# Kernel optimization log

Measured on AMD Instinct MI355X. Metric: run time of the kernel, lower is better.

The kernel has to match this reference:

```python
import jax, jax.numpy as jnp
import numpy as np

B, L, H, D = 4, 2048, 12, 64
CHUNK = 128  # chunk size for the causal linear-attention scan
EPS = 1e-6


def setup_inputs() -> dict:
    key = jax.random.key(0)
    kq, kk, kv = jax.random.split(key, 3)
    return {
        "q": jax.random.normal(kq, (B, L, H, D), jnp.float32),
        "k": jax.random.normal(kk, (B, L, H, D), jnp.float32),
        "v": jax.random.normal(kv, (B, L, H, D), jnp.float32),
    }


def _phi(x):
    # elu feature map: elu(x) + 1 (strictly positive)
    return jax.nn.elu(x) + 1.0


def _causal_linear(q, k, v):
    """Chunked causal linear attention numerator.
    out[l] = q[l] @ sum_{s<=l} k[s] (x) v[s].  q,k,v: [N,L,H,D]."""
    n, l, h, d = q.shape
    g = l // CHUNK
    qc = q.reshape(n, g, CHUNK, h, d)
    kc = k.reshape(n, g, CHUNK, h, d)
    vc = v.reshape(n, g, CHUNK, h, d)
    # per-chunk kv outer-product sums -> [N, G, H, D, M]
    kv = jnp.einsum('ngchd,ngchm->nghdm', kc, vc)
    # exclusive prefix sum over chunks (state entering each chunk)
    s_incl = jnp.cumsum(kv, axis=1)
    s_excl = jnp.concatenate([jnp.zeros_like(s_incl[:, :1]), s_incl[:, :-1]], axis=1)
    inter = jnp.einsum('ngchd,nghdm->ngchm', qc, s_excl)
    # intra-chunk causal part
    scores = jnp.einsum('ngchd,ngshd->ngchs', qc, kc)  # [N,G,C,H,C]
    mask = jnp.tril(jnp.ones((CHUNK, CHUNK), scores.dtype))  # s <= c
    scores = scores * mask.reshape(1, 1, CHUNK, 1, CHUNK)
    intra = jnp.einsum('ngchs,ngshm->ngchm', scores, vc)
    return (inter + intra).reshape(n, l, h, -1)


def reference(q, k, v):
    qf = _phi(q)
    kf = _phi(k)
    # normalizer z[n,l,h] = q[l] . cumsum_s<=l k[s]
    z = jnp.einsum('nlhd,nlhd->nlh', qf, jnp.cumsum(kf, axis=1)) + EPS
    num = _causal_linear(qf, kf, v)
    return num / z[..., None]
```

## Files before the change

kernel.cpp:

```cpp
#include <hip/hip_runtime.h>

#define NB 4
#define LL 2048
#define NH 12
#define DD 64
#define CB 128
#define NG (LL/CB)
#define NBH (NB*NH)
#define ST_BYTES (DD*DD*2)
#define KS_BASE_BYTES ((size_t)NBH*NG*ST_BYTES)

typedef short bf16x8 __attribute__((ext_vector_type(8)));
typedef float f32x4  __attribute__((ext_vector_type(4)));

#define SWZ8(row, x)  ((x) ^ (((row) & 7) << 4))
#define SWZ16(row, x) ((x) ^ (((row) & 15) << 4))

__device__ __forceinline__ float phi(float x) {
    return x > 0.0f ? x + 1.0f : __expf(x);
}
__device__ __forceinline__ unsigned f2bf1(float x) {
    union { float f; unsigned u; } v; v.f = x;
    return (v.u + 0x7FFFu + ((v.u >> 16) & 1u)) >> 16;
}
__device__ __forceinline__ unsigned packbf(float a, float b) {
    return f2bf1(a) | (f2bf1(b) << 16);
}
__device__ __forceinline__ float bf2f(unsigned short u) {
    union { unsigned u; float f; } v; v.u = ((unsigned)u) << 16; return v.f;
}
__device__ __forceinline__ void addbf8(float* run, uint4 a) {
    const unsigned u[4] = {a.x, a.y, a.z, a.w};
    #pragma unroll
    for (int i = 0; i < 4; ++i) {
        run[2*i+0] += bf2f((unsigned short)(u[i] & 0xffffu));
        run[2*i+1] += bf2f((unsigned short)(u[i] >> 16));
    }
}
__device__ __forceinline__ uint4 pack8(const float* run) {
    uint4 s;
    s.x = packbf(run[0], run[1]); s.y = packbf(run[2], run[3]);
    s.z = packbf(run[4], run[5]); s.w = packbf(run[6], run[7]);
    return s;
}

__global__ __launch_bounds__(256) void la_chunk_sums(
    const float* __restrict__ kin, const float* __restrict__ vin,
    char* __restrict__ wsb)
{
    __shared__ __align__(16) char sm[32768];
    const int bid = blockIdx.x;
    const int g = bid & (NG-1);
    const int h = (bid >> 4) % NH;
    const int n = bid / (NG*NH);
    const int t = threadIdx.x;
    const int l0 = g * CB;
    const int w = t >> 6, l = t & 63, gq = l >> 4, c16 = l & 15;

    #pragma unroll
    for (int p = 0; p < 8; ++p) {
        const int i = p*256 + t;
        const int r = i >> 4, c4 = i & 15;
        const size_t gidx = ((size_t)((n*LL + l0 + r)*NH + h))*DD + c4*4;
        float4 kk = *(const float4*)(kin + gidx);
        float4 vl = *(const float4*)(vin + gidx);
        const float kf[4] = {phi(kk.x), phi(kk.y), phi(kk.z), phi(kk.w)};
        const float vf[4] = {vl.x, vl.y, vl.z, vl.w};
        #pragma unroll
        for (int j = 0; j < 4; ++j) {
            const int d = c4*4 + j;
            *(unsigned short*)(sm +         d*256 + SWZ16(d, 2*r)) = (unsigned short)f2bf1(kf[j]);
            *(unsigned short*)(sm + 16384 + d*256 + SWZ16(d, 2*r)) = (unsigned short)f2bf1(vf[j]);
        }
    }
    __syncthreads();

    const int m = 16*w + c16;
    bf16x8 va[4];
    #pragma unroll
    for (int ks = 0; ks < 4; ++ks)
        va[ks] = *(const bf16x8*)(sm + 16384 + m*256 + SWZ16(m, 64*ks + 16*gq));
    const short one = (short)0x3F80;
    const bf16x8 ones = {one, one, one, one, one, one, one, one};

    f32x4 acc[4], ksa[4];
    #pragma unroll
    for (int td = 0; td < 4; ++td) {
        acc[td][0]=0.f; acc[td][1]=0.f; acc[td][2]=0.f; acc[td][3]=0.f;
        ksa[td][0]=0.f; ksa[td][1]=0.f; ksa[td][2]=0.f; ksa[td][3]=0.f;
    }
    #pragma unroll
    for (int td = 0; td < 4; ++td) {
        const int d = 16*td + c16;
        #pragma unroll
        for (int ks = 0; ks < 4; ++ks) {
            const bf16x8 kb = *(const bf16x8*)(sm + d*256 + SWZ16(d, 64*ks + 16*gq));
            acc[td] = __builtin_amdgcn_mfma_f32_16x16x32_bf16(va[ks], kb, acc[td], 0, 0, 0);
            ksa[td] = __builtin_amdgcn_mfma_f32_16x16x32_bf16(ones,  kb, ksa[td], 0, 0, 0);
        }
    }
    __syncthreads();

    #pragma unroll
    for (int td = 0; td < 4; ++td)
        #pragma unroll
        for (int e = 0; e < 4; ++e) {
            const int mr = 16*w + 4*gq + e;
            const int d  = 16*td + c16;
            *(unsigned short*)(sm + mr*128 + SWZ8(mr, 2*d)) = (unsigned short)f2bf1(acc[td][e]);
        }
    if (w == 0 && gq == 0) {
        float* ksw = (float*)(wsb + KS_BASE_BYTES) + (size_t)((n*NH + h)*NG + g)*DD;
        #pragma unroll
        for (int td = 0; td < 4; ++td)
            ksw[16*td + c16] = ksa[td][0];
    }
    __syncthreads();

    char* stg = wsb + (size_t)((n*NH + h)*NG + g)*ST_BYTES;
    #pragma unroll
    for (int p = 0; p < 2; ++p) {
        const int i = p*256 + t;
        const int mr = i >> 3, cc = i & 7;
        *(uint4*)(stg + mr*128 + cc*16) = *(const uint4*)(sm + mr*128 + SWZ8(mr, cc*16));
    }
}

__global__ __launch_bounds__(256) void la_scan(char* __restrict__ wsb)
{
    const int nh = blockIdx.x / 3;
    const int sl = blockIdx.x % 3;
    const int t  = threadIdx.x;
    if (sl < 2) {
        const int t4 = sl*256 + t;
        char* base = wsb + (size_t)nh * NG * ST_BYTES + (size_t)t4 * 16;
        float run[8];
        #pragma unroll
        for (int i = 0; i < 8; ++i) run[i] = 0.f;
        #pragma unroll
        for (int g2 = 0; g2 < NG; g2 += 2) {
            uint4 a0 = *(uint4*)(base + (size_t)(g2+0)*ST_BYTES);
            uint4 a1 = *(uint4*)(base + (size_t)(g2+1)*ST_BYTES);
            *(uint4*)(base + (size_t)(g2+0)*ST_BYTES) = pack8(run);
            addbf8(run, a0);
            *(uint4*)(base + (size_t)(g2+1)*ST_BYTES) = pack8(run);
            addbf8(run, a1);
        }
    } else if (t < DD) {
        float* base = (float*)(wsb + KS_BASE_BYTES) + (size_t)nh * NG * DD + t;
        float run = 0.f;
        #pragma unroll
        for (int g4 = 0; g4 < NG; g4 += 4) {
            float a0 = base[(g4+0)*DD], a1 = base[(g4+1)*DD];
            float a2 = base[(g4+2)*DD], a3 = base[(g4+3)*DD];
            base[(g4+0)*DD] = run; run += a0;
            base[(g4+1)*DD] = run; run += a1;
            base[(g4+2)*DD] = run; run += a2;
            base[(g4+3)*DD] = run; run += a3;
        }
    }
}

#define SM_Q   0
#define SM_K   16384
#define SM_S   0
#define SM_VT  32768
#define SM_STX 49152
#define SM_KSX 57344
#define SM_ZL  57600
#define SM_BYTES 58112

__global__ __launch_bounds__(512) void la_output(
    const float* __restrict__ qin, const float* __restrict__ kin,
    const float* __restrict__ vin, const char* __restrict__ wsb,
    float* __restrict__ out)
{
    __shared__ __align__(16) char sm[SM_BYTES];
    const int bid = blockIdx.x;
    const int g = bid & (NG-1);
    const int h = (bid >> 4) % NH;
    const int n = bid / (NG*NH);
    const int t = threadIdx.x;
    const int l0 = g * CB;
    const int w = t >> 6, l = t & 63, gq = l >> 4, c16 = l & 15;
    const int c = 16*w + c16;

    #pragma unroll
    for (int p = 0; p < 4; ++p) {
        const int i = p*512 + t;
        const int r = i >> 4, c4 = i & 15;
        const size_t gidx = ((size_t)((n*LL + l0 + r)*NH + h))*DD + c4*4;
        float4 qq = *(const float4*)(qin + gidx);
        float4 kk = *(const float4*)(kin + gidx);
        float4 vl = *(const float4*)(vin + gidx);
        uint2 qp; qp.x = packbf(phi(qq.x), phi(qq.y)); qp.y = packbf(phi(qq.z), phi(qq.w));
        uint2 kp; kp.x = packbf(phi(kk.x), phi(kk.y)); kp.y = packbf(phi(kk.z), phi(kk.w));
        *(uint2*)(sm + SM_Q + r*128 + SWZ8(r, c4*8)) = qp;
        *(uint2*)(sm + SM_K + r*128 + SWZ8(r, c4*8)) = kp;
        const float vf[4] = {vl.x, vl.y, vl.z, vl.w};
        #pragma unroll
        for (int j = 0; j < 4; ++j) {
            const int m = c4*4 + j;
            *(unsigned short*)(sm + SM_VT + m*256 + SWZ16(m, 2*r)) = (unsigned short)f2bf1(vf[j]);
        }
    }
    {
        const char* stg = wsb + (size_t)((n*NH + h)*NG + g)*ST_BYTES;
        const int mr = t >> 3, cc = t & 7;
        *(uint4*)(sm + SM_STX + mr*128 + SWZ8(mr, cc*16)) = *(const uint4*)(stg + mr*128 + cc*16);
    }
    if (t < DD)
        ((float*)(sm + SM_KSX))[t] =
            ((const float*)(wsb + KS_BASE_BYTES))[(size_t)((n*NH + h)*NG + g)*DD + t];
    __syncthreads();

    const bf16x8 qf0 = *(const bf16x8*)(sm + SM_Q + c*128 + SWZ8(c, 16*gq));
    const bf16x8 qf1 = *(const bf16x8*)(sm + SM_Q + c*128 + SWZ8(c, 64 + 16*gq));

    f32x4 sreg[8];
    #pragma unroll
    for (int tr = 0; tr < 8; ++tr) {
        const int r = 16*tr + c16;
        const bf16x8 ka0 = *(const bf16x8*)(sm + SM_K + r*128 + SWZ8(r, 16*gq));
        const bf16x8 ka1 = *(const bf16x8*)(sm + SM_K + r*128 + SWZ8(r, 64 + 16*gq));
        f32x4 a; a[0]=0.f; a[1]=0.f; a[2]=0.f; a[3]=0.f;
        a = __builtin_amdgcn_mfma_f32_16x16x32_bf16(ka0, qf0, a, 0, 0, 0);
        a = __builtin_amdgcn_mfma_f32_16x16x32_bf16(ka1, qf1, a, 0, 0, 0);
        sreg[tr] = a;
    }
    float z = 0.f;
    #pragma unroll
    for (int tr = 0; tr < 8; ++tr)
        #pragma unroll
        for (int e = 0; e < 4; ++e) {
            const int rr = 16*tr + 4*gq + e;
            if (rr <= c) z += sreg[tr][e]; else sreg[tr][e] = 0.f;
        }
    {
        const float* ksxf = (const float*)(sm + SM_KSX);
        #pragma unroll
        for (int i = 0; i < 8; ++i) {
            z += bf2f((unsigned short)qf0[i]) * ksxf[8*gq + i];
            z += bf2f((unsigned short)qf1[i]) * ksxf[32 + 8*gq + i];
        }
    }
    z += __shfl_xor(z, 16);
    z += __shfl_xor(z, 32);
    __syncthreads();

    #pragma unroll
    for (int tr = 0; tr < 8; ++tr) {
        uint2 sp; sp.x = packbf(sreg[tr][0], sreg[tr][1]); sp.y = packbf(sreg[tr][2], sreg[tr][3]);
        *(uint2*)(sm + SM_S + c*256 + SWZ16(c, 32*tr + 8*gq)) = sp;
    }
    if (gq == 0) ((float*)(sm + SM_ZL))[c] = z;
    __syncthreads();

    bf16x8 sf[4];
    #pragma unroll
    for (int ks = 0; ks < 4; ++ks)
        sf[ks] = *(const bf16x8*)(sm + SM_S + c*256 + SWZ16(c, 64*ks + 16*gq));
    f32x4 acc[4];
    #pragma unroll
    for (int tm = 0; tm < 4; ++tm) { acc[tm][0]=0.f; acc[tm][1]=0.f; acc[tm][2]=0.f; acc[tm][3]=0.f; }
    #pragma unroll
    for (int tm = 0; tm < 4; ++tm) {
        const int m = 16*tm + c16;
        #pragma unroll
        for (int ks = 0; ks < 4; ++ks) {
            const bf16x8 vf = *(const bf16x8*)(sm + SM_VT + m*256 + SWZ16(m, 64*ks + 16*gq));
            acc[tm] = __builtin_amdgcn_mfma_f32_16x16x32_bf16(sf[ks], vf, acc[tm], 0, 0, 0);
        }
        const bf16x8 st0 = *(const bf16x8*)(sm + SM_STX + m*128 + SWZ8(m, 16*gq));
        const bf16x8 st1 = *(const bf16x8*)(sm + SM_STX + m*128 + SWZ8(m, 64 + 16*gq));
        acc[tm] = __builtin_amdgcn_mfma_f32_16x16x32_bf16(qf0, st0, acc[tm], 0, 0, 0);
        acc[tm] = __builtin_amdgcn_mfma_f32_16x16x32_bf16(qf1, st1, acc[tm], 0, 0, 0);
    }

    float zinv[4];
    #pragma unroll
    for (int e = 0; e < 4; ++e) {
        const float zr = ((const float*)(sm + SM_ZL))[16*w + 4*gq + e];
        zinv[e] = 1.0f / (zr + 1e-6f);
    }
    #pragma unroll
    for (int tm = 0; tm < 4; ++tm)
        #pragma unroll
        for (int e = 0; e < 4; ++e) {
            const int cr = 16*w + 4*gq + e;
            const int m  = 16*tm + c16;
            out[((size_t)((n*LL + l0 + cr)*NH + h))*DD + m] = acc[tm][e] * zinv[e];
        }
}

extern "C" void kernel_launch(void* const* d_in, const int* in_sizes, int n_in,
                              void* d_out, int out_size, void* d_ws, size_t ws_size,
                              hipStream_t stream) {
    const float* q = (const float*)d_in[0];
    const float* k = (const float*)d_in[1];
    const float* v = (const float*)d_in[2];
    float* out = (float*)d_out;
    char* wsb  = (char*)d_ws;

    const int nblk = NB * NH * NG;
    la_chunk_sums<<<nblk, 256, 0, stream>>>(k, v, wsb);
    la_scan<<<NBH*3, 256, 0, stream>>>(wsb);
    la_output<<<nblk, 512, 0, stream>>>(q, k, v, wsb, out);
}
```

Measured before the change: 40.94 us.

## Skip fully masked score tiles and drop block barriers in output kernel

Splits the intra-chunk score computation into two 64-row halves, and waves whose query rows all lie below 64 skip the fully masked upper half. Each wave now writes its scores into its own rows of the Q shared-memory region, using only wave barriers, which removes two block-wide __syncthreads and the separate score buffer. The normalizer is passed between lanes with shuffles instead of shared memory, and the inter-chunk state is loaded straight from global memory into registers. Shared memory shrinks and the launch bounds request 6 blocks per CU to raise occupancy, at the cost of more register pressure from the preloaded state fragments.

```diff
diff --git a/kernel.cpp b/kernel.cpp
--- a/kernel.cpp
+++ b/kernel.cpp
@@ -163,14 +163,11 @@
 
 #define SM_Q   0
 #define SM_K   16384
-#define SM_S   0
 #define SM_VT  32768
-#define SM_STX 49152
-#define SM_KSX 57344
-#define SM_ZL  57600
-#define SM_BYTES 58112
-
-__global__ __launch_bounds__(512) void la_output(
+#define SM_KSX 49152
+#define SM_BYTES 49408
+
+__global__ __launch_bounds__(512, 6) void la_output(
     const float* __restrict__ qin, const float* __restrict__ kin,
     const float* __restrict__ vin, const char* __restrict__ wsb,
     float* __restrict__ out)
@@ -204,38 +201,34 @@
             *(unsigned short*)(sm + SM_VT + m*256 + SWZ16(m, 2*r)) = (unsigned short)f2bf1(vf[j]);
         }
     }
-    {
-        const char* stg = wsb + (size_t)((n*NH + h)*NG + g)*ST_BYTES;
-        const int mr = t >> 3, cc = t & 7;
-        *(uint4*)(sm + SM_STX + mr*128 + SWZ8(mr, cc*16)) = *(const uint4*)(stg + mr*128 + cc*16);
-    }
     if (t < DD)
         ((float*)(sm + SM_KSX))[t] =
             ((const float*)(wsb + KS_BASE_BYTES))[(size_t)((n*NH + h)*NG + g)*DD + t];
+
+    const char* stg = wsb + (size_t)((n*NH + h)*NG + g)*ST_BYTES;
+    bf16x8 stf[4][2];
+    #pragma unroll
+    for (int tm = 0; tm < 4; ++tm) {
+        const int m = 16*tm + c16;
+        stf[tm][0] = *(const bf16x8*)(stg + m*128 +      16*gq);
+        stf[tm][1] = *(const bf16x8*)(stg + m*128 + 64 + 16*gq);
+    }
     __syncthreads();
 
     const bf16x8 qf0 = *(const bf16x8*)(sm + SM_Q + c*128 + SWZ8(c, 16*gq));
     const bf16x8 qf1 = *(const bf16x8*)(sm + SM_Q + c*128 + SWZ8(c, 64 + 16*gq));
 
-    f32x4 sreg[8];
-    #pragma unroll
-    for (int tr = 0; tr < 8; ++tr) {
-        const int r = 16*tr + c16;
-        const bf16x8 ka0 = *(const bf16x8*)(sm + SM_K + r*128 + SWZ8(r, 16*gq));
-        const bf16x8 ka1 = *(const bf16x8*)(sm + SM_K + r*128 + SWZ8(r, 64 + 16*gq));
-        f32x4 a; a[0]=0.f; a[1]=0.f; a[2]=0.f; a[3]=0.f;
-        a = __builtin_amdgcn_mfma_f32_16x16x32_bf16(ka0, qf0, a, 0, 0, 0);
-        a = __builtin_amdgcn_mfma_f32_16x16x32_bf16(ka1, qf1, a, 0, 0, 0);
-        sreg[tr] = a;
-    }
+    f32x4 acc[4];
+    #pragma unroll
+    for (int tm = 0; tm < 4; ++tm) { acc[tm][0]=0.f; acc[tm][1]=0.f; acc[tm][2]=0.f; acc[tm][3]=0.f; }
+
+    #pragma unroll
+    for (int tm = 0; tm < 4; ++tm) {
+        acc[tm] = __builtin_amdgcn_mfma_f32_16x16x32_bf16(qf0, stf[tm][0], acc[tm], 0, 0, 0);
+        acc[tm] = __builtin_amdgcn_mfma_f32_16x16x32_bf16(qf1, stf[tm][1], acc[tm], 0, 0, 0);
+    }
+
     float z = 0.f;
-    #pragma unroll
-    for (int tr = 0; tr < 8; ++tr)
-        #pragma unroll
-        for (int e = 0; e < 4; ++e) {
-            const int rr = 16*tr + 4*gq + e;
-            if (rr <= c) z += sreg[tr][e]; else sreg[tr][e] = 0.f;
-        }
     {
         const float* ksxf = (const float*)(sm + SM_KSX);
         #pragma unroll
@@ -244,45 +237,58 @@
             z += bf2f((unsigned short)qf1[i]) * ksxf[32 + 8*gq + i];
         }
     }
+
+    #pragma unroll
+    for (int h2 = 0; h2 < 2; ++h2) {
+        if (h2 == 0 || w >= 4) {
+            f32x4 sreg[4];
+            #pragma unroll
+            for (int tr4 = 0; tr4 < 4; ++tr4) {
+                const int r = 64*h2 + 16*tr4 + c16;
+                const bf16x8 ka0 = *(const bf16x8*)(sm + SM_K + r*128 + SWZ8(r, 16*gq));
+                const bf16x8 ka1 = *(const bf16x8*)(sm + SM_K + r*128 + SWZ8(r, 64 + 16*gq));
+                f32x4 a; a[0]=0.f; a[1]=0.f; a[2]=0.f; a[3]=0.f;
+                a = __builtin_amdgcn_mfma_f32_16x16x32_bf16(ka0, qf0, a, 0, 0, 0);
+                a = __builtin_amdgcn_mfma_f32_16x16x32_bf16(ka1, qf1, a, 0, 0, 0);
+                sreg[tr4] = a;
+            }
+            #pragma unroll
+            for (int tr4 = 0; tr4 < 4; ++tr4)
+                #pragma unroll
+                for (int e = 0; e < 4; ++e) {
+                    const int rr = 64*h2 + 16*tr4 + 4*gq + e;
+                    if (rr <= c) z += sreg[tr4][e]; else sreg[tr4][e] = 0.f;
+                }
+            #pragma unroll
+            for (int tr4 = 0; tr4 < 4; ++tr4) {
+                uint2 sp; sp.x = packbf(sreg[tr4][0], sreg[tr4][1]);
+                          sp.y = packbf(sreg[tr4][2], sreg[tr4][3]);
+                *(uint2*)(sm + SM_Q + c*128 + SWZ8(c, 32*tr4 + 8*gq)) = sp;
+            }
+            __builtin_amdgcn_wave_barrier();
+            const bf16x8 sf0 = *(const bf16x8*)(sm + SM_Q + c*128 + SWZ8(c, 16*gq));
+            const bf16x8 sf1 = *(const bf16x8*)(sm + SM_Q + c*128 + SWZ8(c, 64 + 16*gq));
+            #pragma unroll
+            for (int tm = 0; tm < 4; ++tm) {
+                const int m = 16*tm + c16;
+                const bf16x8 vf0 = *(const bf16x8*)(sm + SM_VT + m*256 + SWZ16(m, 64*(2*h2+0) + 16*gq));
+                const bf16x8 vf1 = *(const bf16x8*)(sm + SM_VT + m*256 + SWZ16(m, 64*(2*h2+1) + 16*gq));
+                acc[tm] = __builtin_amdgcn_mfma_f32_16x16x32_bf16(sf0, vf0, acc[tm], 0, 0, 0);
+                acc[tm] = __builtin_amdgcn_mfma_f32_16x16x32_bf16(sf1, vf1, acc[tm], 0, 0, 0);
+            }
+            __builtin_amdgcn_wave_barrier();
+        }
+    }
+
     z += __shfl_xor(z, 16);
     z += __shfl_xor(z, 32);
-    __syncthreads();
-
-    #pragma unroll
-    for (int tr = 0; tr < 8; ++tr) {
-        uint2 sp; sp.x = packbf(sreg[tr][0], sreg[tr][1]); sp.y = packbf(sreg[tr][2], sreg[tr][3]);
-        *(uint2*)(sm + SM_S + c*256 + SWZ16(c, 32*tr + 8*gq)) = sp;
-    }
-    if (gq == 0) ((float*)(sm + SM_ZL))[c] = z;
-    __syncthreads();
-
-    bf16x8 sf[4];
-    #pragma unroll
-    for (int ks = 0; ks < 4; ++ks)
-        sf[ks] = *(const bf16x8*)(sm + SM_S + c*256 + SWZ16(c, 64*ks + 16*gq));
-    f32x4 acc[4];
-    #pragma unroll
-    for (int tm = 0; tm < 4; ++tm) { acc[tm][0]=0.f; acc[tm][1]=0.f; acc[tm][2]=0.f; acc[tm][3]=0.f; }
-    #pragma unroll
-    for (int tm = 0; tm < 4; ++tm) {
-        const int m = 16*tm + c16;
-        #pragma unroll
-        for (int ks = 0; ks < 4; ++ks) {
-            const bf16x8 vf = *(const bf16x8*)(sm + SM_VT + m*256 + SWZ16(m, 64*ks + 16*gq));
-            acc[tm] = __builtin_amdgcn_mfma_f32_16x16x32_bf16(sf[ks], vf, acc[tm], 0, 0, 0);
-        }
-        const bf16x8 st0 = *(const bf16x8*)(sm + SM_STX + m*128 + SWZ8(m, 16*gq));
-        const bf16x8 st1 = *(const bf16x8*)(sm + SM_STX + m*128 + SWZ8(m, 64 + 16*gq));
-        acc[tm] = __builtin_amdgcn_mfma_f32_16x16x32_bf16(qf0, st0, acc[tm], 0, 0, 0);
-        acc[tm] = __builtin_amdgcn_mfma_f32_16x16x32_bf16(qf1, st1, acc[tm], 0, 0, 0);
-    }
-
     float zinv[4];
     #pragma unroll
     for (int e = 0; e < 4; ++e) {
-        const float zr = ((const float*)(sm + SM_ZL))[16*w + 4*gq + e];
+        const float zr = __shfl(z, 4*gq + e, 16);
         zinv[e] = 1.0f / (zr + 1e-6f);
     }
+
     #pragma unroll
     for (int tm = 0; tm < 4; ++tm)
         #pragma unroll
```

After: 41.55 us. About the same (+1.5%).
